# Kernel tuning notes

Hardware: AMD Instinct MI355X
Metric: run time of the kernel (lower is better)

The kernel has to match this reference:

```python
import jax, jax.numpy as jnp
from jax import lax
import numpy as np

B, N, C = 16, 4096, 81          # batch, rois, classes (incl. background)
VARIANCES = np.array([0.1, 0.1, 0.2, 0.2], dtype=np.float32)
MAX_TOTAL = 200                  # max_total_size (= per-class cap here)
K = 200                          # per-class candidates kept before NMS
SCORE_TH = 0.5
IOU_TH = 0.5                     # tf combined NMS default
EPS = 1e-8


def setup_inputs() -> dict:
    key = jax.random.key(0)
    k1, k2, k3, k4 = jax.random.split(key, 4)
    yx = jax.random.uniform(k1, (B, N, 2)) * 0.8
    hw = 0.05 + jax.random.uniform(k2, (B, N, 2)) * 0.15
    roi_bboxes = jnp.concatenate([yx, yx + hw], axis=-1)          # [B,N,4] y1x1y2x2 in [0,1]
    pred_deltas = jax.random.normal(k3, (B, N, C * 4)) * 0.5      # [B,N,C*4]
    logits = jax.random.normal(k4, (B, N, C)) * 3.0
    pred_label_probs = jax.nn.softmax(logits, axis=-1)            # [B,N,C]
    return {"roi_bboxes": roi_bboxes, "pred_deltas": pred_deltas,
            "pred_label_probs": pred_label_probs}


def delta_to_bbox(anchors, deltas):
    # anchors [...,4] y1,x1,y2,x2 ; deltas [...,4] dy,dx,dh,dw
    ah = anchors[..., 2] - anchors[..., 0]
    aw = anchors[..., 3] - anchors[..., 1]
    acy = anchors[..., 0] + 0.5 * ah
    acx = anchors[..., 1] + 0.5 * aw
    bh = jnp.exp(deltas[..., 2]) * ah
    bw = jnp.exp(deltas[..., 3]) * aw
    bcy = deltas[..., 0] * ah + acy
    bcx = deltas[..., 1] * aw + acx
    y1 = bcy - 0.5 * bh
    x1 = bcx - 0.5 * bw
    return jnp.stack([y1, x1, y1 + bh, x1 + bw], axis=-1)


def pairwise_iou(boxes):  # [K,4] -> [K,K]
    y1 = jnp.maximum(boxes[:, None, 0], boxes[None, :, 0])
    x1 = jnp.maximum(boxes[:, None, 1], boxes[None, :, 1])
    y2 = jnp.minimum(boxes[:, None, 2], boxes[None, :, 2])
    x2 = jnp.minimum(boxes[:, None, 3], boxes[None, :, 3])
    inter = jnp.maximum(y2 - y1, 0.0) * jnp.maximum(x2 - x1, 0.0)
    area = jnp.maximum(boxes[:, 2] - boxes[:, 0], 0.0) * jnp.maximum(boxes[:, 3] - boxes[:, 1], 0.0)
    union = area[:, None] + area[None, :] - inter
    return inter / (union + EPS)


def _nms_keep(boxes_k, scores_k):
    # boxes_k [K,4] sorted by score desc; greedy suppression mask
    ious = pairwise_iou(boxes_k)
    rng = jnp.arange(K)
    valid = scores_k > SCORE_TH

    def step(keep, i):
        sup = (ious[i] > IOU_TH) & (rng > i) & keep[i]
        return keep & ~sup, None

    keep, _ = lax.scan(step, valid, rng)
    return keep


def _per_class(boxes_c, scores_c):
    # boxes_c [N,4], scores_c [N] -> top-K candidates + NMS-kept scores
    sc, idx = lax.top_k(scores_c, K)
    bx = boxes_c[idx]                       # [K,4]
    keep = _nms_keep(bx, sc)
    return bx, jnp.where(keep, sc, 0.0)


def _per_image(boxes_b, scores_b):
    # boxes_b [N,C,4], scores_b [N,C]
    bx, sc = jax.vmap(_per_class, in_axes=(1, 1))(boxes_b, scores_b)  # [C,K,4],[C,K]
    top_sc, top_idx = lax.top_k(sc.reshape(-1), MAX_TOTAL)
    top_bx = bx.reshape(-1, 4)[top_idx]
    top_lbl = (top_idx // K).astype(jnp.float32)
    valid = top_sc > 0.0
    top_bx = jnp.clip(jnp.where(valid[:, None], top_bx, 0.0), 0.0, 1.0)  # clip_boxes=True
    return top_bx, jnp.where(valid, top_sc, 0.0), jnp.where(valid, top_lbl, 0.0)


def reference(roi_bboxes, pred_deltas, pred_label_probs):
    b, n, _ = roi_bboxes.shape
    c = pred_label_probs.shape[-1]
    deltas = pred_deltas.reshape(b, n, c, 4) * jnp.asarray(VARIANCES)
    pred_bboxes = delta_to_bbox(roi_bboxes[:, :, None, :], deltas)       # [B,N,C,4]
    bg = jnp.argmax(pred_label_probs, axis=-1) == 0                      # background mask
    scores = jnp.where(bg[..., None], 0.0, pred_label_probs)             # [B,N,C]
    final_bboxes, final_scores, final_labels = jax.vmap(_per_image)(pred_bboxes, scores)
    return final_bboxes, final_labels, final_scores
```

## Files before the change

kernel.cpp:

```cpp
#include <hip/hip_runtime.h>
#include <math.h>

#pragma clang fp contract(off)

constexpr int NB  = 16;
constexpr int NR  = 4096;
constexpr int NC  = 81;
constexpr int KK  = 200;
constexpr int CAP = 4096;
constexpr int ROWS_PER_BLK = 64;
constexpr int CHUNKS = NR / ROWS_PER_BLK;
constexpr int GRID = NB * NR / ROWS_PER_BLK;
constexpr int MAXC = 1024;
constexpr int TCHUNK = 256;
constexpr int NCHUNK = CAP / TCHUNK;
constexpr float SCORE_TH = 0.5f;
constexpr float IOU_TH   = 0.5f;
constexpr float EPSF     = 1e-8f;

struct SK { float s; int key; };

__device__ __forceinline__ void decode_box(const float4& a, const float4& d,
                                           float& y1, float& x1, float& y2, float& x2) {
    float ah  = a.z - a.x;
    float aw  = a.w - a.y;
    float acy = a.x + 0.5f * ah;
    float acx = a.y + 0.5f * aw;
    float dy = d.x * 0.1f, dx = d.y * 0.1f;
    float dh = d.z * 0.2f, dw = d.w * 0.2f;
    float bh  = expf(dh) * ah;
    float bw  = expf(dw) * aw;
    float bcy = dy * ah + acy;
    float bcx = dx * aw + acx;
    y1 = bcy - 0.5f * bh;
    x1 = bcx - 0.5f * bw;
    y2 = y1 + bh;
    x2 = x1 + bw;
}

__global__ void k_classify(const float* __restrict__ roi,
                           const float* __restrict__ deltas,
                           const float* __restrict__ probs,
                           int* __restrict__ blk_cnt,
                           int* __restrict__ final_count,
                           int* __restrict__ scls,
                           float2* __restrict__ ssr,
                           float4* __restrict__ sbox) {
    __shared__ float lp[ROWS_PER_BLK * NC];
    __shared__ int wcnt[4], wbase[4];
    const int bid = blockIdx.x, tid = threadIdx.x;

    const float4* src = (const float4*)(probs + (size_t)bid * ROWS_PER_BLK * NC);
    float4* dst = (float4*)lp;
    for (int v = tid; v < ROWS_PER_BLK * NC / 4; v += 256) dst[v] = src[v];
    __syncthreads();

    int g = tid >> 2;
    int j = tid & 3;
    const float* row = lp + g * NC;
    float m = -1.0f;
    int am = 127;
    for (int c = j; c < NC; c += 4) {
        float v = row[c];
        if (v > m) { m = v; am = c; }
    }
    for (int mask = 1; mask <= 2; mask <<= 1) {
        float om = __shfl_xor(m, mask);
        int   oi = __shfl_xor(am, mask);
        if (om > m || (om == m && oi < am)) { m = om; am = oi; }
    }

    bool pred = (j == 0) && (am != 0) && (m > SCORE_TH);
    unsigned long long bal = __ballot(pred);
    int lane = tid & 63, w = tid >> 6;
    if (lane == 0) wcnt[w] = __popcll(bal);
    __syncthreads();
    if (tid == 0) {
        int run = 0;
        for (int i = 0; i < 4; ++i) { wbase[i] = run; run += wcnt[i]; }
        blk_cnt[bid] = run;
        if ((bid & (CHUNKS - 1)) == 0) final_count[bid / CHUNKS] = 0;
    }
    __syncthreads();

    if (pred) {
        int pos = wbase[w] + __popcll(bal & ((1ull << lane) - 1ull));
        int r = bid * ROWS_PER_BLK + g;
        float4 a = ((const float4*)roi)[r];
        float4 d = *(const float4*)(deltas + ((size_t)r * NC + am) * 4);
        float y1, x1, y2, x2;
        decode_box(a, d, y1, x1, y2, x2);
        int idx = bid * ROWS_PER_BLK + pos;
        scls[idx] = am;
        ssr[idx]  = make_float2(m, (float)(r & (NR - 1)));
        sbox[idx] = make_float4(y1, x1, y2, x2);
    }
}

__global__ void k_perclass(const int* __restrict__ blk_cnt,
                           const int* __restrict__ scls,
                           const float2* __restrict__ ssr,
                           const float4* __restrict__ sbox,
                           int* __restrict__ final_count,
                           float4* __restrict__ fbox,
                           SK* __restrict__ sk) {
    __shared__ int ccnt[CHUNKS];
    __shared__ int lcnt;
    __shared__ float ls[MAXC], lroi[MAXC];
    __shared__ unsigned short lidx[MAXC];
    __shared__ float ss[KK], sy1[KK], sx1[KK], sy2[KK], sx2[KK], sar[KK];
    __shared__ unsigned long long sup[KK][4];
    __shared__ int skeep[KK];
    __shared__ int sbase;

    int b = blockIdx.x / NC, c = blockIdx.x % NC;
    if (c == 0) return;
    const int tid = threadIdx.x;

    if (tid < CHUNKS) ccnt[tid] = blk_cnt[b * CHUNKS + tid];
    if (tid == 0) lcnt = 0;
    __syncthreads();

    const int* sc = scls + (size_t)b * NR;
    const float2* sr = ssr + (size_t)b * NR;
    for (int sidx = tid; sidx < NR; sidx += 256) {
        int chunk = sidx >> 6, s = sidx & 63;
        if (s < ccnt[chunk] && sc[sidx] == c) {
            int p = atomicAdd(&lcnt, 1);
            if (p < MAXC) {
                float2 v = sr[sidx];
                ls[p] = v.x; lroi[p] = v.y; lidx[p] = (unsigned short)sidx;
            }
        }
    }
    __syncthreads();
    int Mc = lcnt; if (Mc > MAXC) Mc = MAXC;
    if (Mc == 0) return;

    for (int i = tid; i < Mc; i += 256) {
        float si = ls[i], ri = lroi[i];
        int rank = 0;
        for (int jj = 0; jj < Mc; ++jj) {
            float sj = ls[jj], rj = lroi[jj];
            rank += (int)((sj > si) | ((sj == si) & (rj < ri)));
        }
        if (rank < KK) {
            float4 bx = sbox[(size_t)b * NR + lidx[i]];
            ss[rank] = si;
            sy1[rank] = bx.x; sx1[rank] = bx.y; sy2[rank] = bx.z; sx2[rank] = bx.w;
            sar[rank] = fmaxf(bx.z - bx.x, 0.f) * fmaxf(bx.w - bx.y, 0.f);
        }
    }
    __syncthreads();

    int L = Mc < KK ? Mc : KK;

    for (int idx = tid; idx < L * 4; idx += 256) {
        int i = idx >> 2, w = idx & 3;
        int j0 = w * 64;
        unsigned long long bits = 0;
        int jend = j0 + 64 < L ? j0 + 64 : L;
        int jstart = j0 > i + 1 ? j0 : i + 1;
        if (jstart < jend) {
            float yi1 = sy1[i], xi1 = sx1[i], yi2 = sy2[i], xi2 = sx2[i], ai = sar[i];
            for (int j = jstart; j < jend; ++j) {
                float yy1 = fmaxf(yi1, sy1[j]), xx1 = fmaxf(xi1, sx1[j]);
                float yy2 = fminf(yi2, sy2[j]), xx2 = fminf(xi2, sx2[j]);
                float inter = fmaxf(yy2 - yy1, 0.f) * fmaxf(xx2 - xx1, 0.f);
                float uni = ai + sar[j] - inter;
                if (inter / (uni + EPSF) > IOU_TH) bits |= 1ull << (j - j0);
            }
        }
        sup[i][w] = bits;
    }
    __syncthreads();

    if (tid < 64) {
        int lane = tid;
        int kmask = 0;
        #pragma unroll
        for (int s = 0; s < 4; ++s) if (s * 64 + lane < L) kmask |= 1 << s;
        for (int i = 0; i < L; ++i) {
            int oi = i & 63, si = i >> 6;
            unsigned long long r0 = sup[i][0], r1 = sup[i][1];
            unsigned long long r2 = sup[i][2], r3 = sup[i][3];
            int keep_i = (__shfl(kmask, oi) >> si) & 1;
            if (keep_i) {
                int supb = (int)((r0 >> lane) & 1)
                         | ((int)((r1 >> lane) & 1) << 1)
                         | ((int)((r2 >> lane) & 1) << 2)
                         | ((int)((r3 >> lane) & 1) << 3);
                kmask &= ~supb;
            }
        }
        #pragma unroll
        for (int s = 0; s < 4; ++s) {
            int jj = s * 64 + lane;
            if (jj < L) skeep[jj] = (kmask >> s) & 1;
        }
    }
    __syncthreads();

    if (tid == 0) {
        int tot = 0;
        for (int i = 0; i < L; ++i) tot += skeep[i];
        sbase = atomicAdd(&final_count[b], tot);
    }
    __syncthreads();
    int base = sbase;

    for (int i = tid; i < L; i += 256) {
        if (skeep[i]) {
            int pos = 0;
            for (int j = 0; j < i; ++j) pos += skeep[j];
            int slot = base + pos;
            if (slot < CAP) {
                fbox[(size_t)b * CAP + slot] = make_float4(sy1[i], sx1[i], sy2[i], sx2[i]);
                sk[(size_t)b * CAP + slot].s = ss[i];
                sk[(size_t)b * CAP + slot].key = c * KK + i;
            }
        }
    }
}

__global__ void k_topk(const int* __restrict__ final_count,
                       const float4* __restrict__ fbox,
                       const SK* __restrict__ sk,
                       float* __restrict__ out) {
    int b = blockIdx.x / NCHUNK, chunk = blockIdx.x % NCHUNK;
    int M = final_count[b];
    if (M > CAP) M = CAP;

    float* obox = out + (size_t)b * KK * 4;
    float* olbl = out + (size_t)NB * KK * 4 + (size_t)b * KK;
    float* osc  = out + (size_t)NB * KK * 5 + (size_t)b * KK;

    if (chunk == 0) {
        int Mi = M < KK ? M : KK;
        for (int i = Mi + (int)threadIdx.x; i < KK; i += blockDim.x) {
            obox[i * 4 + 0] = 0.f; obox[i * 4 + 1] = 0.f;
            obox[i * 4 + 2] = 0.f; obox[i * 4 + 3] = 0.f;
            olbl[i] = 0.f; osc[i] = 0.f;
        }
    }
    if (chunk * TCHUNK >= M) return;

    __shared__ SK sL[CAP];
    const float2* src = (const float2*)(sk + (size_t)b * CAP);
    float2* dstv = (float2*)sL;
    for (int i = threadIdx.x; i < M; i += blockDim.x) dstv[i] = src[i];
    __syncthreads();

    int e = chunk * TCHUNK + threadIdx.x;
    if (e >= M) return;
    float se = sL[e].s; int ke = sL[e].key;
    int rank = 0;
    const float4* p4 = (const float4*)sL;
    int npair = M >> 1;
    #pragma unroll 4
    for (int p = 0; p < npair; ++p) {
        float4 v = p4[p];
        int k0 = __float_as_int(v.y), k1 = __float_as_int(v.w);
        rank += (int)((v.x > se) | ((v.x == se) & (k0 < ke)));
        rank += (int)((v.z > se) | ((v.z == se) & (k1 < ke)));
    }
    if (M & 1) {
        float sj = sL[M - 1].s; int kj = sL[M - 1].key;
        rank += (int)((sj > se) | ((sj == se) & (kj < ke)));
    }
    if (rank < KK) {
        float4 bx = fbox[(size_t)b * CAP + e];
        obox[rank * 4 + 0] = fminf(fmaxf(bx.x, 0.f), 1.f);
        obox[rank * 4 + 1] = fminf(fmaxf(bx.y, 0.f), 1.f);
        obox[rank * 4 + 2] = fminf(fmaxf(bx.z, 0.f), 1.f);
        obox[rank * 4 + 3] = fminf(fmaxf(bx.w, 0.f), 1.f);
        olbl[rank] = (float)(ke / KK);
        osc[rank]  = se;
    }
}

extern "C" void kernel_launch(void* const* d_in, const int* in_sizes, int n_in,
                              void* d_out, int out_size, void* d_ws, size_t ws_size,
                              hipStream_t stream) {
    const float* roi    = (const float*)d_in[0];
    const float* deltas = (const float*)d_in[1];
    const float* probs  = (const float*)d_in[2];
    float* out = (float*)d_out;

    char* base = (char*)d_ws;
    int*    blk_cnt     = (int*)base;
    int*    final_count = (int*)(base + 4096);
    int*    scls        = (int*)(base + 8192);
    float2* ssr         = (float2*)(base + 8192 + 262144);
    float4* sbox        = (float4*)(base + 8192 + 262144 + 524288);
    float4* fbox        = (float4*)(base + 8192 + 262144 + 524288 + 1048576);
    SK*     sk          = (SK*)(base + 8192 + 262144 + 524288 + 1048576 + 1048576);

    k_classify<<<GRID, 256, 0, stream>>>(roi, deltas, probs, blk_cnt, final_count,
                                         scls, ssr, sbox);
    k_perclass<<<NB * NC, 256, 0, stream>>>(blk_cnt, scls, ssr, sbox,
                                            final_count, fbox, sk);
    k_topk<<<NB * NCHUNK, 256, 0, stream>>>(final_count, fbox, sk, out);
}
```

Baseline: 72.37 us.

## Fuse classification into per-class NMS kernel with per-class output segments

Removes the separate classify kernel. Each per-class block now scans its own probability column directly, treating p > 0.5 as the foreground test, and decodes boxes only for the top-K candidates. Per-class results go to fixed segments with a count array instead of a global atomic append, and top-k rebuilds a prefix sum and binary-searches to gather candidates. This saves a kernel launch and intermediate buffers. In exchange, every block does strided column reads across the whole batch's probability tensor, so the same cache lines are re-read about 80 times.

```diff
diff --git a/kernel.cpp b/kernel.cpp
--- a/kernel.cpp
+++ b/kernel.cpp
@@ -6,11 +6,9 @@
 constexpr int NB  = 16;
 constexpr int NR  = 4096;
 constexpr int NC  = 81;
+constexpr int NCM1 = NC - 1;
 constexpr int KK  = 200;
 constexpr int CAP = 4096;
-constexpr int ROWS_PER_BLK = 64;
-constexpr int CHUNKS = NR / ROWS_PER_BLK;
-constexpr int GRID = NB * NR / ROWS_PER_BLK;
 constexpr int MAXC = 1024;
 constexpr int TCHUNK = 256;
 constexpr int NCHUNK = CAP / TCHUNK;
@@ -20,135 +18,69 @@
 
 struct SK { float s; int key; };
 
-__device__ __forceinline__ void decode_box(const float4& a, const float4& d,
-                                           float& y1, float& x1, float& y2, float& x2) {
-    float ah  = a.z - a.x;
-    float aw  = a.w - a.y;
-    float acy = a.x + 0.5f * ah;
-    float acx = a.y + 0.5f * aw;
-    float dy = d.x * 0.1f, dx = d.y * 0.1f;
-    float dh = d.z * 0.2f, dw = d.w * 0.2f;
-    float bh  = expf(dh) * ah;
-    float bw  = expf(dw) * aw;
-    float bcy = dy * ah + acy;
-    float bcx = dx * aw + acx;
-    y1 = bcy - 0.5f * bh;
-    x1 = bcx - 0.5f * bw;
-    y2 = y1 + bh;
-    x2 = x1 + bw;
-}
-
-__global__ void k_classify(const float* __restrict__ roi,
+__global__ void k_perclass(const float* __restrict__ probs,
+                           const float* __restrict__ roi,
                            const float* __restrict__ deltas,
-                           const float* __restrict__ probs,
-                           int* __restrict__ blk_cnt,
-                           int* __restrict__ final_count,
-                           int* __restrict__ scls,
-                           float2* __restrict__ ssr,
-                           float4* __restrict__ sbox) {
-    __shared__ float lp[ROWS_PER_BLK * NC];
-    __shared__ int wcnt[4], wbase[4];
-    const int bid = blockIdx.x, tid = threadIdx.x;
-
-    const float4* src = (const float4*)(probs + (size_t)bid * ROWS_PER_BLK * NC);
-    float4* dst = (float4*)lp;
-    for (int v = tid; v < ROWS_PER_BLK * NC / 4; v += 256) dst[v] = src[v];
-    __syncthreads();
-
-    int g = tid >> 2;
-    int j = tid & 3;
-    const float* row = lp + g * NC;
-    float m = -1.0f;
-    int am = 127;
-    for (int c = j; c < NC; c += 4) {
-        float v = row[c];
-        if (v > m) { m = v; am = c; }
-    }
-    for (int mask = 1; mask <= 2; mask <<= 1) {
-        float om = __shfl_xor(m, mask);
-        int   oi = __shfl_xor(am, mask);
-        if (om > m || (om == m && oi < am)) { m = om; am = oi; }
-    }
-
-    bool pred = (j == 0) && (am != 0) && (m > SCORE_TH);
-    unsigned long long bal = __ballot(pred);
-    int lane = tid & 63, w = tid >> 6;
-    if (lane == 0) wcnt[w] = __popcll(bal);
-    __syncthreads();
-    if (tid == 0) {
-        int run = 0;
-        for (int i = 0; i < 4; ++i) { wbase[i] = run; run += wcnt[i]; }
-        blk_cnt[bid] = run;
-        if ((bid & (CHUNKS - 1)) == 0) final_count[bid / CHUNKS] = 0;
-    }
-    __syncthreads();
-
-    if (pred) {
-        int pos = wbase[w] + __popcll(bal & ((1ull << lane) - 1ull));
-        int r = bid * ROWS_PER_BLK + g;
-        float4 a = ((const float4*)roi)[r];
-        float4 d = *(const float4*)(deltas + ((size_t)r * NC + am) * 4);
-        float y1, x1, y2, x2;
-        decode_box(a, d, y1, x1, y2, x2);
-        int idx = bid * ROWS_PER_BLK + pos;
-        scls[idx] = am;
-        ssr[idx]  = make_float2(m, (float)(r & (NR - 1)));
-        sbox[idx] = make_float4(y1, x1, y2, x2);
-    }
-}
-
-__global__ void k_perclass(const int* __restrict__ blk_cnt,
-                           const int* __restrict__ scls,
-                           const float2* __restrict__ ssr,
-                           const float4* __restrict__ sbox,
-                           int* __restrict__ final_count,
-                           float4* __restrict__ fbox,
-                           SK* __restrict__ sk) {
-    __shared__ int ccnt[CHUNKS];
-    __shared__ int lcnt;
+                           int* __restrict__ kcnt,
+                           SK* __restrict__ sk_seg,
+                           float4* __restrict__ fbox_seg) {
+    __shared__ int   lcnt;
     __shared__ float ls[MAXC], lroi[MAXC];
-    __shared__ unsigned short lidx[MAXC];
     __shared__ float ss[KK], sy1[KK], sx1[KK], sy2[KK], sx2[KK], sar[KK];
     __shared__ unsigned long long sup[KK][4];
-    __shared__ int skeep[KK];
-    __shared__ int sbase;
-
-    int b = blockIdx.x / NC, c = blockIdx.x % NC;
-    if (c == 0) return;
-    const int tid = threadIdx.x;
-
-    if (tid < CHUNKS) ccnt[tid] = blk_cnt[b * CHUNKS + tid];
+    __shared__ int   skeep[KK];
+
+    const int bid = blockIdx.x, tid = threadIdx.x;
+    const int b = bid / NCM1, cm1 = bid % NCM1, c = cm1 + 1;
+
     if (tid == 0) lcnt = 0;
     __syncthreads();
 
-    const int* sc = scls + (size_t)b * NR;
-    const float2* sr = ssr + (size_t)b * NR;
-    for (int sidx = tid; sidx < NR; sidx += 256) {
-        int chunk = sidx >> 6, s = sidx & 63;
-        if (s < ccnt[chunk] && sc[sidx] == c) {
-            int p = atomicAdd(&lcnt, 1);
-            if (p < MAXC) {
-                float2 v = sr[sidx];
-                ls[p] = v.x; lroi[p] = v.y; lidx[p] = (unsigned short)sidx;
-            }
-        }
-    }
-    __syncthreads();
-    int Mc = lcnt; if (Mc > MAXC) Mc = MAXC;
-    if (Mc == 0) return;
+    const float* pcol = probs + (size_t)b * NR * NC + c;
+    #pragma unroll 4
+    for (int r = tid; r < NR; r += 256) {
+        float p = pcol[(size_t)r * NC];
+        if (p > SCORE_TH) {
+            int q = atomicAdd(&lcnt, 1);
+            if (q < MAXC) { ls[q] = p; lroi[q] = (float)r; }
+        }
+    }
+    __syncthreads();
+
+    int Mc = lcnt < MAXC ? lcnt : MAXC;
+    if (Mc == 0) {
+        if (tid == 0) kcnt[b * NCM1 + cm1] = 0;
+        return;
+    }
 
     for (int i = tid; i < Mc; i += 256) {
         float si = ls[i], ri = lroi[i];
         int rank = 0;
-        for (int jj = 0; jj < Mc; ++jj) {
-            float sj = ls[jj], rj = lroi[jj];
+        for (int j = 0; j < Mc; ++j) {
+            float sj = ls[j], rj = lroi[j];
             rank += (int)((sj > si) | ((sj == si) & (rj < ri)));
         }
         if (rank < KK) {
-            float4 bx = sbox[(size_t)b * NR + lidx[i]];
+            int r = (int)ri;
+            float4 a = ((const float4*)roi)[(size_t)b * NR + r];
+            float4 d = *(const float4*)(deltas + (((size_t)b * NR + r) * NC + c) * 4);
+            float ah  = a.z - a.x;
+            float aw  = a.w - a.y;
+            float acy = a.x + 0.5f * ah;
+            float acx = a.y + 0.5f * aw;
+            float dy = d.x * 0.1f, dx = d.y * 0.1f;
+            float dh = d.z * 0.2f, dw = d.w * 0.2f;
+            float bh  = expf(dh) * ah;
+            float bw  = expf(dw) * aw;
+            float bcy = dy * ah + acy;
+            float bcx = dx * aw + acx;
+            float y1 = bcy - 0.5f * bh;
+            float x1 = bcx - 0.5f * bw;
+            float y2 = y1 + bh;
+            float x2 = x1 + bw;
             ss[rank] = si;
-            sy1[rank] = bx.x; sx1[rank] = bx.y; sy2[rank] = bx.z; sx2[rank] = bx.w;
-            sar[rank] = fmaxf(bx.z - bx.x, 0.f) * fmaxf(bx.w - bx.y, 0.f);
+            sy1[rank] = y1; sx1[rank] = x1; sy2[rank] = y2; sx2[rank] = x2;
+            sar[rank] = fmaxf(y2 - y1, 0.f) * fmaxf(x2 - x1, 0.f);
         }
     }
     __syncthreads();
@@ -201,35 +133,42 @@
     }
     __syncthreads();
 
-    if (tid == 0) {
-        int tot = 0;
-        for (int i = 0; i < L; ++i) tot += skeep[i];
-        sbase = atomicAdd(&final_count[b], tot);
-    }
-    __syncthreads();
-    int base = sbase;
-
     for (int i = tid; i < L; i += 256) {
         if (skeep[i]) {
             int pos = 0;
             for (int j = 0; j < i; ++j) pos += skeep[j];
-            int slot = base + pos;
-            if (slot < CAP) {
-                fbox[(size_t)b * CAP + slot] = make_float4(sy1[i], sx1[i], sy2[i], sx2[i]);
-                sk[(size_t)b * CAP + slot].s = ss[i];
-                sk[(size_t)b * CAP + slot].key = c * KK + i;
-            }
-        }
+            size_t idx = ((size_t)b * NC + c) * KK + pos;
+            sk_seg[idx].s = ss[i];
+            sk_seg[idx].key = c * KK + i;
+            fbox_seg[idx] = make_float4(sy1[i], sx1[i], sy2[i], sx2[i]);
+        }
+    }
+    if (tid == 0) {
+        int tot = 0;
+        for (int i = 0; i < L; ++i) tot += skeep[i];
+        kcnt[b * NCM1 + cm1] = tot;
     }
 }
 
-__global__ void k_topk(const int* __restrict__ final_count,
-                       const float4* __restrict__ fbox,
-                       const SK* __restrict__ sk,
+__global__ void k_topk(const int* __restrict__ kcnt,
+                       const SK* __restrict__ sk_seg,
+                       const float4* __restrict__ fbox_seg,
                        float* __restrict__ out) {
     int b = blockIdx.x / NCHUNK, chunk = blockIdx.x % NCHUNK;
-    int M = final_count[b];
-    if (M > CAP) M = CAP;
+    const int tid = threadIdx.x;
+
+    __shared__ int pfx[NCM1 + 1];
+    __shared__ SK  sL[CAP];
+
+    if (tid < NCM1) pfx[tid + 1] = kcnt[b * NCM1 + tid];
+    if (tid == 0) pfx[0] = 0;
+    __syncthreads();
+    if (tid == 0) {
+        int run = 0;
+        for (int s = 1; s <= NCM1; ++s) { run += pfx[s]; pfx[s] = run; }
+    }
+    __syncthreads();
+    int M = pfx[NCM1];
 
     float* obox = out + (size_t)b * KK * 4;
     float* olbl = out + (size_t)NB * KK * 4 + (size_t)b * KK;
@@ -237,7 +176,7 @@
 
     if (chunk == 0) {
         int Mi = M < KK ? M : KK;
-        for (int i = Mi + (int)threadIdx.x; i < KK; i += blockDim.x) {
+        for (int i = Mi + tid; i < KK; i += 256) {
             obox[i * 4 + 0] = 0.f; obox[i * 4 + 1] = 0.f;
             obox[i * 4 + 2] = 0.f; obox[i * 4 + 3] = 0.f;
             olbl[i] = 0.f; osc[i] = 0.f;
@@ -245,13 +184,19 @@
     }
     if (chunk * TCHUNK >= M) return;
 
-    __shared__ SK sL[CAP];
-    const float2* src = (const float2*)(sk + (size_t)b * CAP);
-    float2* dstv = (float2*)sL;
-    for (int i = threadIdx.x; i < M; i += blockDim.x) dstv[i] = src[i];
-    __syncthreads();
-
-    int e = chunk * TCHUNK + threadIdx.x;
+    for (int i = tid; i < M; i += 256) {
+        int lo = 0, hi = NCM1;
+        while (lo + 1 < hi + 1) {
+            int mid = (lo + hi + 1) >> 1;
+            if (pfx[mid] <= i) lo = mid; else hi = mid - 1;
+        }
+        int cseg = lo + 1;
+        int k = i - pfx[lo];
+        sL[i] = sk_seg[((size_t)b * NC + cseg) * KK + k];
+    }
+    __syncthreads();
+
+    int e = chunk * TCHUNK + tid;
     if (e >= M) return;
     float se = sL[e].s; int ke = sL[e].key;
     int rank = 0;
@@ -269,7 +214,7 @@
         rank += (int)((sj > se) | ((sj == se) & (kj < ke)));
     }
     if (rank < KK) {
-        float4 bx = fbox[(size_t)b * CAP + e];
+        float4 bx = fbox_seg[(size_t)b * NC * KK + ke];
         obox[rank * 4 + 0] = fminf(fmaxf(bx.x, 0.f), 1.f);
         obox[rank * 4 + 1] = fminf(fmaxf(bx.y, 0.f), 1.f);
         obox[rank * 4 + 2] = fminf(fmaxf(bx.z, 0.f), 1.f);
@@ -288,17 +233,11 @@
     float* out = (float*)d_out;
 
     char* base = (char*)d_ws;
-    int*    blk_cnt     = (int*)base;
-    int*    final_count = (int*)(base + 4096);
-    int*    scls        = (int*)(base + 8192);
-    float2* ssr         = (float2*)(base + 8192 + 262144);
-    float4* sbox        = (float4*)(base + 8192 + 262144 + 524288);
-    float4* fbox        = (float4*)(base + 8192 + 262144 + 524288 + 1048576);
-    SK*     sk          = (SK*)(base + 8192 + 262144 + 524288 + 1048576 + 1048576);
-
-    k_classify<<<GRID, 256, 0, stream>>>(roi, deltas, probs, blk_cnt, final_count,
-                                         scls, ssr, sbox);
-    k_perclass<<<NB * NC, 256, 0, stream>>>(blk_cnt, scls, ssr, sbox,
-                                            final_count, fbox, sk);
-    k_topk<<<NB * NCHUNK, 256, 0, stream>>>(final_count, fbox, sk, out);
+    int*    kcnt     = (int*)base;
+    SK*     sk_seg   = (SK*)(base + 8192);
+    float4* fbox_seg = (float4*)(base + 8192 + 2073600);
+
+    k_perclass<<<NB * NCM1, 256, 0, stream>>>(probs, roi, deltas,
+                                              kcnt, sk_seg, fbox_seg);
+    k_topk<<<NB * NCHUNK, 256, 0, stream>>>(kcnt, sk_seg, fbox_seg, out);
 }
```

Measured after the change: 82.12 us. 13.5% more time.

## Replace atomic compaction of per-class survivors with fixed segments and prefix sums

Applied to the files above, without the earlier changes.

Each per-class block now writes its kept candidates into a fixed per-class segment and records a count, instead of reserving a slot in a per-image buffer through an atomicAdd. The top-k kernel builds a prefix sum over the class counts and gathers candidates with a binary search. Boxes are fetched by key at the end. This removes the atomic and the zeroing of the final count in the classify kernel, and also skips launching blocks for the background class. In exchange every top-k block does redundant prefix and gather work.

```diff
diff --git a/kernel.cpp b/kernel.cpp
--- a/kernel.cpp
+++ b/kernel.cpp
@@ -6,6 +6,7 @@
 constexpr int NB  = 16;
 constexpr int NR  = 4096;
 constexpr int NC  = 81;
+constexpr int NCM1 = NC - 1;
 constexpr int KK  = 200;
 constexpr int CAP = 4096;
 constexpr int ROWS_PER_BLK = 64;
@@ -42,7 +43,6 @@
                            const float* __restrict__ deltas,
                            const float* __restrict__ probs,
                            int* __restrict__ blk_cnt,
-                           int* __restrict__ final_count,
                            int* __restrict__ scls,
                            float2* __restrict__ ssr,
                            float4* __restrict__ sbox) {
@@ -79,7 +79,6 @@
         int run = 0;
         for (int i = 0; i < 4; ++i) { wbase[i] = run; run += wcnt[i]; }
         blk_cnt[bid] = run;
-        if ((bid & (CHUNKS - 1)) == 0) final_count[bid / CHUNKS] = 0;
     }
     __syncthreads();
 
@@ -101,9 +100,9 @@
                            const int* __restrict__ scls,
                            const float2* __restrict__ ssr,
                            const float4* __restrict__ sbox,
-                           int* __restrict__ final_count,
-                           float4* __restrict__ fbox,
-                           SK* __restrict__ sk) {
+                           int* __restrict__ kcnt,
+                           SK* __restrict__ sk_seg,
+                           float4* __restrict__ fbox_seg) {
     __shared__ int ccnt[CHUNKS];
     __shared__ int lcnt;
     __shared__ float ls[MAXC], lroi[MAXC];
@@ -111,11 +110,9 @@
     __shared__ float ss[KK], sy1[KK], sx1[KK], sy2[KK], sx2[KK], sar[KK];
     __shared__ unsigned long long sup[KK][4];
     __shared__ int skeep[KK];
-    __shared__ int sbase;
-
-    int b = blockIdx.x / NC, c = blockIdx.x % NC;
-    if (c == 0) return;
-    const int tid = threadIdx.x;
+
+    const int bid = blockIdx.x, tid = threadIdx.x;
+    const int b = bid / NCM1, cm1 = bid % NCM1, c = cm1 + 1;
 
     if (tid < CHUNKS) ccnt[tid] = blk_cnt[b * CHUNKS + tid];
     if (tid == 0) lcnt = 0;
@@ -134,8 +131,11 @@
         }
     }
     __syncthreads();
-    int Mc = lcnt; if (Mc > MAXC) Mc = MAXC;
-    if (Mc == 0) return;
+    int Mc = lcnt < MAXC ? lcnt : MAXC;
+    if (Mc == 0) {
+        if (tid == 0) kcnt[bid] = 0;
+        return;
+    }
 
     for (int i = tid; i < Mc; i += 256) {
         float si = ls[i], ri = lroi[i];
@@ -201,35 +201,42 @@
     }
     __syncthreads();
 
-    if (tid == 0) {
-        int tot = 0;
-        for (int i = 0; i < L; ++i) tot += skeep[i];
-        sbase = atomicAdd(&final_count[b], tot);
-    }
-    __syncthreads();
-    int base = sbase;
-
     for (int i = tid; i < L; i += 256) {
         if (skeep[i]) {
             int pos = 0;
             for (int j = 0; j < i; ++j) pos += skeep[j];
-            int slot = base + pos;
-            if (slot < CAP) {
-                fbox[(size_t)b * CAP + slot] = make_float4(sy1[i], sx1[i], sy2[i], sx2[i]);
-                sk[(size_t)b * CAP + slot].s = ss[i];
-                sk[(size_t)b * CAP + slot].key = c * KK + i;
-            }
-        }
-    }
-}
-
-__global__ void k_topk(const int* __restrict__ final_count,
-                       const float4* __restrict__ fbox,
-                       const SK* __restrict__ sk,
+            size_t segbase = (size_t)bid * KK;
+            sk_seg[segbase + pos].s = ss[i];
+            sk_seg[segbase + pos].key = c * KK + i;
+            fbox_seg[segbase + i] = make_float4(sy1[i], sx1[i], sy2[i], sx2[i]);
+        }
+    }
+    if (tid == 0) {
+        int tot = 0;
+        for (int i = 0; i < L; ++i) tot += skeep[i];
+        kcnt[bid] = tot;
+    }
+}
+
+__global__ void k_topk(const int* __restrict__ kcnt,
+                       const SK* __restrict__ sk_seg,
+                       const float4* __restrict__ fbox_seg,
                        float* __restrict__ out) {
     int b = blockIdx.x / NCHUNK, chunk = blockIdx.x % NCHUNK;
-    int M = final_count[b];
-    if (M > CAP) M = CAP;
+    const int tid = threadIdx.x;
+
+    __shared__ int pfx[NCM1 + 1];
+    __shared__ SK  sL[CAP];
+
+    if (tid < NCM1) pfx[tid + 1] = kcnt[b * NCM1 + tid];
+    if (tid == 0) pfx[0] = 0;
+    __syncthreads();
+    if (tid == 0) {
+        int run = 0;
+        for (int s = 1; s <= NCM1; ++s) { run += pfx[s]; pfx[s] = run; }
+    }
+    __syncthreads();
+    int M = pfx[NCM1];
 
     float* obox = out + (size_t)b * KK * 4;
     float* olbl = out + (size_t)NB * KK * 4 + (size_t)b * KK;
@@ -237,7 +244,7 @@
 
     if (chunk == 0) {
         int Mi = M < KK ? M : KK;
-        for (int i = Mi + (int)threadIdx.x; i < KK; i += blockDim.x) {
+        for (int i = Mi + tid; i < KK; i += 256) {
             obox[i * 4 + 0] = 0.f; obox[i * 4 + 1] = 0.f;
             obox[i * 4 + 2] = 0.f; obox[i * 4 + 3] = 0.f;
             olbl[i] = 0.f; osc[i] = 0.f;
@@ -245,13 +252,18 @@
     }
     if (chunk * TCHUNK >= M) return;
 
-    __shared__ SK sL[CAP];
-    const float2* src = (const float2*)(sk + (size_t)b * CAP);
-    float2* dstv = (float2*)sL;
-    for (int i = threadIdx.x; i < M; i += blockDim.x) dstv[i] = src[i];
-    __syncthreads();
-
-    int e = chunk * TCHUNK + threadIdx.x;
+    for (int i = tid; i < M; i += 256) {
+        int lo = 0, hi = NCM1 - 1;
+        while (lo < hi) {
+            int mid = (lo + hi + 1) >> 1;
+            if (pfx[mid] <= i) lo = mid; else hi = mid - 1;
+        }
+        int k = i - pfx[lo];
+        sL[i] = sk_seg[((size_t)b * NCM1 + lo) * KK + k];
+    }
+    __syncthreads();
+
+    int e = chunk * TCHUNK + tid;
     if (e >= M) return;
     float se = sL[e].s; int ke = sL[e].key;
     int rank = 0;
@@ -269,7 +281,8 @@
         rank += (int)((sj > se) | ((sj == se) & (kj < ke)));
     }
     if (rank < KK) {
-        float4 bx = fbox[(size_t)b * CAP + e];
+        int cm1 = ke / KK - 1, ipre = ke % KK;
+        float4 bx = fbox_seg[((size_t)b * NCM1 + cm1) * KK + ipre];
         obox[rank * 4 + 0] = fminf(fmaxf(bx.x, 0.f), 1.f);
         obox[rank * 4 + 1] = fminf(fmaxf(bx.y, 0.f), 1.f);
         obox[rank * 4 + 2] = fminf(fmaxf(bx.z, 0.f), 1.f);
@@ -288,17 +301,17 @@
     float* out = (float*)d_out;
 
     char* base = (char*)d_ws;
-    int*    blk_cnt     = (int*)base;
-    int*    final_count = (int*)(base + 4096);
-    int*    scls        = (int*)(base + 8192);
-    float2* ssr         = (float2*)(base + 8192 + 262144);
-    float4* sbox        = (float4*)(base + 8192 + 262144 + 524288);
-    float4* fbox        = (float4*)(base + 8192 + 262144 + 524288 + 1048576);
-    SK*     sk          = (SK*)(base + 8192 + 262144 + 524288 + 1048576 + 1048576);
-
-    k_classify<<<GRID, 256, 0, stream>>>(roi, deltas, probs, blk_cnt, final_count,
+    int*    blk_cnt  = (int*)base;
+    int*    kcnt     = (int*)(base + 4096);
+    int*    scls     = (int*)(base + 16384);
+    float2* ssr      = (float2*)(base + 16384 + 262144);
+    float4* sbox     = (float4*)(base + 16384 + 262144 + 524288);
+    SK*     sk_seg   = (SK*)(base + 16384 + 262144 + 524288 + 1048576);
+    float4* fbox_seg = (float4*)(base + 16384 + 262144 + 524288 + 1048576 + 2097152);
+
+    k_classify<<<GRID, 256, 0, stream>>>(roi, deltas, probs, blk_cnt,
                                          scls, ssr, sbox);
-    k_perclass<<<NB * NC, 256, 0, stream>>>(blk_cnt, scls, ssr, sbox,
-                                            final_count, fbox, sk);
-    k_topk<<<NB * NCHUNK, 256, 0, stream>>>(final_count, fbox, sk, out);
-}
+    k_perclass<<<NB * NCM1, 256, 0, stream>>>(blk_cnt, scls, ssr, sbox,
+                                              kcnt, sk_seg, fbox_seg);
+    k_topk<<<NB * NCHUNK, 256, 0, stream>>>(kcnt, sk_seg, fbox_seg, out);
+}
```

After: 69.22 us. 4.3% less time.
